# Optimization experiments

Hardware: AMD Instinct MI355X
Metric: run time of the kernel (lower is better)

The kernel has to match this reference:

```python
import jax, jax.numpy as jnp
import numpy as np

D_MODEL = 1024
N_HEADS = 16
HEAD_DIM = D_MODEL // N_HEADS


def setup_inputs() -> dict:
    key = jax.random.key(0)
    k1, k2, k3 = jax.random.split(key, 3)
    x = jax.random.normal(k1, (2, 2048, D_MODEL), dtype=jnp.float32)
    w_qkv = jax.random.normal(k2, (3 * D_MODEL, D_MODEL), dtype=jnp.float32) * 0.02
    w_out = jax.random.normal(k3, (D_MODEL, D_MODEL), dtype=jnp.float32) * 0.02
    return {"x": x, "w_qkv": w_qkv, "w_out": w_out}


def reference(x, w_qkv, w_out):
    B, T, D = x.shape
    H, Hd = N_HEADS, HEAD_DIM
    # QKV projection: Linear stores weight as [out, in] -> '...i,oi->...o'
    qkv = jnp.einsum('bti,oi->bto', x, w_qkv)              # [B, T, 3D]
    # split (3*H, Hs) group-major, chunk into q/k/v of H heads each
    qkv = qkv.reshape(B, T, 3, H, Hd)
    q = jnp.transpose(qkv[:, :, 0], (0, 2, 1, 3))          # [B, H, T, Hd]
    k = jnp.transpose(qkv[:, :, 1], (0, 2, 1, 3))
    v = jnp.transpose(qkv[:, :, 2], (0, 2, 1, 3))
    scale = 1.0 / jnp.sqrt(jnp.asarray(Hd, dtype=x.dtype))
    scores = jnp.einsum('bhqd,bhkd->bhqk', q, k) * scale   # [B, H, T, T]
    causal = jnp.tril(jnp.ones((T, T), dtype=bool))        # [T, T]
    scores = jnp.where(causal[None, None], scores, jnp.asarray(-jnp.inf, dtype=scores.dtype))
    attn = jax.nn.softmax(scores, axis=-1)
    ctx = jnp.einsum('bhqk,bhkd->bhqd', attn, v)           # [B, H, T, Hd]
    ctx = jnp.transpose(ctx, (0, 2, 1, 3)).reshape(B, T, D)
    return jnp.einsum('bti,oi->bto', ctx, w_out)
```

## Files before the change

kernel.cpp:

```cpp
#include <hip/hip_runtime.h>


typedef short short8 __attribute__((ext_vector_type(8)));
typedef float f32x4 __attribute__((ext_vector_type(4)));
typedef unsigned short u16;
typedef unsigned int u32;

#define T_SEQ 2048
#define N_B 2
#define N_H 16
#define HD 64
#define DM 1024
#define TRIPLE 3072

__device__ __forceinline__ u16 f2bf(float f) {
  union { float f; unsigned u; } v;
  v.f = f;
  unsigned r = v.u + 0x7fffu + ((v.u >> 16) & 1u);
  return (u16)(r >> 16);
}

__device__ __forceinline__ float bf2f(u16 x) {
  return __uint_as_float((u32)x << 16);
}

__device__ __forceinline__ u32 cvtpk(float a, float b) {
  u32 r;
  asm("v_cvt_pk_bf16_f32 %0, %1, %2" : "=v"(r) : "v"(a), "v"(b));
  return r;
}

typedef const __attribute__((address_space(1))) void gvoid;
typedef __attribute__((address_space(3))) void lvoid;

__device__ __forceinline__ void g2l16(const void* g, void* l) {
  __builtin_amdgcn_global_load_lds((gvoid*)g, (lvoid*)l, 16, 0, 0);
}

__device__ __forceinline__ void storeC(float* p, float v) { *p = v; }
__device__ __forceinline__ void storeC(u16* p, float v) { *p = f2bf(v); }

__global__ __launch_bounds__(256) void cast_all(const float4* __restrict__ x,
                                                const float4* __restrict__ wq,
                                                const float4* __restrict__ wo,
                                                ushort4* __restrict__ out) {
  int i = blockIdx.x * 256 + threadIdx.x;
  const float4* src;
  int off;
  if (i < 1048576) { src = x; off = 0; }
  else if (i < 1835008) { src = wq; off = 1048576; }
  else { src = wo; off = 1835008; }
  float4 v = src[i - off];
  ushort4 o;
  o.x = f2bf(v.x); o.y = f2bf(v.y); o.z = f2bf(v.z); o.w = f2bf(v.w);
  out[i] = o;
}

__global__ __launch_bounds__(256) void vtrans(const u16* __restrict__ qkv,
                                              u16* __restrict__ vT) {
  const int tid = threadIdx.x;
  const int w = tid >> 6, lane = tid & 63;
  const int ti = lane >> 3, di = lane & 7;
  const int h = blockIdx.y, b = blockIdx.z;
  const int t0 = blockIdx.x * 256 + w * 64 + ti * 8;

  const u16* src = qkv + (size_t)(b * T_SEQ + t0) * TRIPLE + 2 * DM + h * HD + di * 8;
  u32 x[8][4];
#pragma unroll
  for (int e = 0; e < 8; ++e) {
    union { short8 v; u32 u[4]; } cv;
    cv.v = *(const short8*)(src + (size_t)e * TRIPLE);
#pragma unroll
    for (int j = 0; j < 4; ++j) x[e][j] = cv.u[j];
  }
  u32 y[8][4];
#pragma unroll
  for (int a = 0; a < 4; ++a)
#pragma unroll
    for (int j = 0; j < 4; ++j) {
      u32 lo = x[2 * a][j], hi = x[2 * a + 1][j];
      y[2 * a][j] = (lo & 0x0000FFFFu) | (hi << 16);
      y[2 * a + 1][j] = (lo >> 16) | (hi & 0xFFFF0000u);
    }
  u16* dst = vT + ((size_t)(b * N_H + h) * HD + di * 8) * T_SEQ + t0;
#pragma unroll
  for (int dd = 0; dd < 8; ++dd) {
    union { short8 v; u32 u[4]; } cv;
#pragma unroll
    for (int a = 0; a < 4; ++a) cv.u[a] = y[2 * a + (dd & 1)][dd >> 1];
    *(short8*)(dst + (size_t)dd * T_SEQ) = cv.v;
  }
}

template <typename OutT>
__global__ __launch_bounds__(256) void gemm_bt(const u16* __restrict__ A,
                                               const u16* __restrict__ W,
                                               OutT* __restrict__ C,
                                               int M, int N, int K) {
  __shared__ char As[128 * 64 * 2];
  __shared__ char Bs[128 * 64 * 2];
  const int tid = threadIdx.x;
  const int lane = tid & 63, w = tid >> 6;
  const int l15 = lane & 15, l4 = lane >> 4;
  const int m0 = blockIdx.y * 128, n0 = blockIdx.x * 128;
  const int wr = (w >> 1) * 64, wc = (w & 1) * 64;

  const f32x4 zero = {0.f, 0.f, 0.f, 0.f};
  f32x4 acc[4][4];
#pragma unroll
  for (int m = 0; m < 4; ++m)
#pragma unroll
    for (int n = 0; n < 4; ++n) acc[m][n] = zero;

  for (int k0 = 0; k0 < K; k0 += 64) {
#pragma unroll
    for (int i = 0; i < 4; ++i) {
      const int cb = (i * 4 + w) * 64;
      const int c = cb + lane;
      const int row = c >> 3;
      const int ks = ((c & 7) ^ (row & 7)) * 8;
      g2l16(A + (size_t)(m0 + row) * K + k0 + ks, As + (size_t)cb * 16);
      g2l16(W + (size_t)(n0 + row) * K + k0 + ks, Bs + (size_t)cb * 16);
    }
    __syncthreads();

#pragma unroll
    for (int kk = 0; kk < 2; ++kk) {
      short8 a[4], b[4];
#pragma unroll
      for (int m = 0; m < 4; ++m) {
        int row = wr + m * 16 + l15;
        int slot = (kk * 4 + l4) ^ (row & 7);
        a[m] = *(const short8*)(As + row * 128 + slot * 16);
      }
#pragma unroll
      for (int n = 0; n < 4; ++n) {
        int row = wc + n * 16 + l15;
        int slot = (kk * 4 + l4) ^ (row & 7);
        b[n] = *(const short8*)(Bs + row * 128 + slot * 16);
      }
#pragma unroll
      for (int m = 0; m < 4; ++m)
#pragma unroll
        for (int n = 0; n < 4; ++n)
          acc[m][n] = __builtin_amdgcn_mfma_f32_16x16x32_bf16(a[m], b[n], acc[m][n], 0, 0, 0);
    }
    __syncthreads();
  }

#pragma unroll
  for (int m = 0; m < 4; ++m)
#pragma unroll
    for (int n = 0; n < 4; ++n)
#pragma unroll
      for (int r = 0; r < 4; ++r) {
        int row = m0 + wr + m * 16 + l4 * 4 + r;
        int col = n0 + wc + n * 16 + l15;
        storeC(C + (size_t)row * N + col, acc[m][n][r]);
      }
}

__global__ __launch_bounds__(256) void attn_fwd(const u16* __restrict__ qkv,
                                                const u16* __restrict__ vT,
                                                u16* __restrict__ ctx) {
  __shared__ char Ks[3][8192];
  __shared__ char Vs[3][8192];
  __shared__ char Pl[4][2048];

  const int tid = threadIdx.x;
  const int lane = tid & 63, w = tid >> 6;
  const int l15 = lane & 15, l4 = lane >> 4;
  const int g = blockIdx.x;
  const int p = blockIdx.y;
  const int h = g & 15, b = g >> 4;
  const int q0A = 64 * p, q0B = 64 * (31 - p);

  const float c_log2 = 0.18033688011112042f;
  short8 qa2[2][2];
#pragma unroll
  for (int ps = 0; ps < 2; ++ps) {
    const int qq0 = ps ? q0B : q0A;
    const u16* qp = qkv + (size_t)(b * T_SEQ + qq0 + w * 16 + l15) * TRIPLE + h * HD;
#pragma unroll
    for (int kk = 0; kk < 2; ++kk) {
      short8 raw = *(const short8*)(qp + kk * 32 + l4 * 8);
      union { short8 v; u32 w4[4]; } qq;
#pragma unroll
      for (int j = 0; j < 4; ++j)
        qq.w4[j] = cvtpk(bf2f((u16)raw[2 * j]) * c_log2,
                         bf2f((u16)raw[2 * j + 1]) * c_log2);
      qa2[ps][kk] = qq.v;
    }
  }

  const int r0 = tid >> 3, c0 = tid & 7;
  const int swz = (c0 ^ (r0 & 7)) << 3;
  const u16* kbase = qkv + (size_t)(b * T_SEQ + r0) * TRIPLE + DM + h * HD + swz;
  const u16* vbase = vT + ((size_t)g * HD + r0) * T_SEQ + swz;

#define STAGE(kt_, buf_)                                                        \
  {                                                                             \
    g2l16(kbase + (size_t)((kt_) * 64) * TRIPLE, Ks[buf_] + tid * 16);          \
    g2l16(kbase + (size_t)((kt_) * 64 + 32) * TRIPLE, Ks[buf_] + tid * 16 + 4096); \
    g2l16(vbase + (u32)((kt_) * 64), Vs[buf_] + tid * 16);                      \
    g2l16(vbase + (size_t)32 * T_SEQ + (u32)((kt_) * 64), Vs[buf_] + tid * 16 + 4096); \
  }

  char* Plb = Pl[w];

  const f32x4 zero = {0.f, 0.f, 0.f, 0.f};
  f32x4 o[4];
#pragma unroll
  for (int nt = 0; nt < 4; ++nt) o[nt] = zero;
  float mr = -INFINITY, lr = 0.f;
  short8 qa0 = qa2[0][0], qa1 = qa2[0][1];
  int q0 = q0A;

  STAGE(0, 0);
  {
    const int kt1 = (1 <= p) ? 1 : 31;
    STAGE(kt1, 1);
  }
  asm volatile("s_waitcnt vmcnt(4)\n\ts_barrier" ::: "memory");

  int cur = 0;
  for (int i = 0;; ++i) {
    const int kt = (i <= p) ? i : 32 - i;

    if (i + 2 <= 32) {
      const int kt2 = (i + 2 <= p) ? i + 2 : 30 - i;
      int sb = cur - 1;
      if (sb < 0) sb = 2;
      STAGE(kt2, sb);
    }

    const int k0 = kt * 64;
    if (k0 <= q0 + w * 16) {
      f32x4 s[4];
#pragma unroll
      for (int mt = 0; mt < 4; ++mt) s[mt] = zero;
      __builtin_amdgcn_s_setprio(1);
#pragma unroll
      for (int mt = 0; mt < 4; ++mt) {
        int row = mt * 16 + l15;
        int slot0 = l4 ^ (row & 7);
        short8 kb0 = *(const short8*)(Ks[cur] + row * 128 + slot0 * 16);
        s[mt] = __builtin_amdgcn_mfma_f32_16x16x32_bf16(kb0, qa0, s[mt], 0, 0, 0);
        int slot1 = (4 + l4) ^ (row & 7);
        short8 kb1 = *(const short8*)(Ks[cur] + row * 128 + slot1 * 16);
        s[mt] = __builtin_amdgcn_mfma_f32_16x16x32_bf16(kb1, qa1, s[mt], 0, 0, 0);
      }
      __builtin_amdgcn_s_setprio(0);

      if (i == p || i == p + 1) {
        const int qrow = q0 + w * 16 + l15;
#pragma unroll
        for (int mt = 0; mt < 4; ++mt)
#pragma unroll
          for (int r = 0; r < 4; ++r) {
            int key = k0 + mt * 16 + l4 * 4 + r;
            if (key > qrow) s[mt][r] = -INFINITY;
          }
      }

      float mx = fmaxf(fmaxf(fmaxf(s[0][0], s[0][1]), fmaxf(s[0][2], s[0][3])),
                       fmaxf(fmaxf(s[1][0], s[1][1]), fmaxf(s[1][2], s[1][3])));
      mx = fmaxf(mx, fmaxf(fmaxf(fmaxf(s[2][0], s[2][1]), fmaxf(s[2][2], s[2][3])),
                           fmaxf(fmaxf(s[3][0], s[3][1]), fmaxf(s[3][2], s[3][3]))));
      mx = fmaxf(mx, __shfl_xor(mx, 16));
      mx = fmaxf(mx, __shfl_xor(mx, 32));
      if (!__all(mx - mr <= 8.0f)) {
        float mn = fmaxf(mr, mx);
        float fr = exp2f(mr - mn);
        lr *= fr;
#pragma unroll
        for (int r = 0; r < 4; ++r) {
          float frq = __shfl(fr, l4 * 4 + r);
#pragma unroll
          for (int nt = 0; nt < 4; ++nt) o[nt][r] *= frq;
        }
        mr = mn;
      }
      float ps = 0.f;
#pragma unroll
      for (int mt = 0; mt < 4; ++mt)
#pragma unroll
        for (int r = 0; r < 4; ++r) {
          float pv = exp2f(s[mt][r] - mr);
          s[mt][r] = pv;
          ps += pv;
        }
      lr += ps;

#pragma unroll
      for (int mt = 0; mt < 4; ++mt) {
        uint2 pw;
        pw.x = cvtpk(s[mt][0], s[mt][1]);
        pw.y = cvtpk(s[mt][2], s[mt][3]);
        int slot = ((mt * 2 + (l4 >> 1)) ^ (l15 & 7));
        *(uint2*)(Plb + l15 * 128 + (slot << 4) + ((l4 & 1) << 3)) = pw;
      }

      __builtin_amdgcn_s_setprio(1);
#pragma unroll
      for (int kk = 0; kk < 2; ++kk) {
        short8 pa = *(const short8*)(Plb + l15 * 128 + (((kk * 4 + l4) ^ (l15 & 7)) << 4));
#pragma unroll
        for (int nt = 0; nt < 4; ++nt) {
          int d = nt * 16 + l15;
          int slot = (kk * 4 + l4) ^ (l15 & 7);
          short8 vb = *(const short8*)(Vs[cur] + d * 128 + slot * 16);
          o[nt] = __builtin_amdgcn_mfma_f32_16x16x32_bf16(pa, vb, o[nt], 0, 0, 0);
        }
      }
      __builtin_amdgcn_s_setprio(0);
    }

    if (i == p || i == 32) {
      lr += __shfl_xor(lr, 16);
      lr += __shfl_xor(lr, 32);
#pragma unroll
      for (int r = 0; r < 4; ++r) {
        float lrq = __shfl(lr, l4 * 4 + r);
        float inv = __builtin_amdgcn_rcpf(lrq);
        size_t t = (size_t)(b * T_SEQ + q0 + w * 16 + l4 * 4 + r);
#pragma unroll
        for (int nt = 0; nt < 4; ++nt)
          ctx[t * DM + h * HD + nt * 16 + l15] = f2bf(o[nt][r] * inv);
      }
      if (i == 32) break;
#pragma unroll
      for (int nt = 0; nt < 4; ++nt) o[nt] = zero;
      mr = -INFINITY; lr = 0.f;
      qa0 = qa2[1][0]; qa1 = qa2[1][1];
      q0 = q0B;
    }

    if (i == 31)
      asm volatile("s_waitcnt vmcnt(0)\n\ts_barrier" ::: "memory");
    else
      asm volatile("s_waitcnt vmcnt(4)\n\ts_barrier" ::: "memory");
    cur = (cur == 2) ? 0 : cur + 1;
  }
#undef STAGE
}

extern "C" void kernel_launch(void* const* d_in, const int* in_sizes, int n_in,
                              void* d_out, int out_size, void* d_ws, size_t ws_size,
                              hipStream_t stream) {
  const float* x = (const float*)d_in[0];
  const float* wqkv = (const float*)d_in[1];
  const float* wout = (const float*)d_in[2];
  float* out = (float*)d_out;
  char* ws = (char*)d_ws;

  u16* xb    = (u16*)(ws);
  u16* wqkvb = (u16*)(ws + 8u * 1024 * 1024);
  u16* woutb = (u16*)(ws + 14u * 1024 * 1024);
  u16* qkvb  = (u16*)(ws + 16u * 1024 * 1024);
  u16* ctxb  = (u16*)(ws + 40u * 1024 * 1024);
  u16* vTb   = (u16*)(ws + 48u * 1024 * 1024);

  cast_all<<<8192, 256, 0, stream>>>((const float4*)x, (const float4*)wqkv,
                                     (const float4*)wout, (ushort4*)xb);

  gemm_bt<u16><<<dim3(24, 32), 256, 0, stream>>>(xb, wqkvb, qkvb, 4096, 3072, 1024);

  vtrans<<<dim3(8, N_H, N_B), 256, 0, stream>>>(qkvb, vTb);

  attn_fwd<<<dim3(32, 16), 256, 0, stream>>>(qkvb, vTb, ctxb);

  gemm_bt<float><<<dim3(8, 32), 256, 0, stream>>>(ctxb, woutb, out, 4096, 1024, 1024);
}
```

Baseline: 130.2 us.

## Double attention tile to 128 queries and keys with 512-thread blocks

Enlarges the attention work tile from 64 to 128 query rows per pass and 128 keys per stage, using 8 waves per block and half the grid in the pair dimension. Each staged K/V tile is now reused by twice as many waves and the loop runs half as many iterations with fewer barriers. The cost is roughly double the LDS per block, more score registers per wave, fewer blocks (less occupancy), and more work wasted at the diagonal tile under the causal mask.

```diff
diff --git a/kernel.cpp b/kernel.cpp
--- a/kernel.cpp
+++ b/kernel.cpp
@@ -160,12 +160,12 @@
       }
 }
 
-__global__ __launch_bounds__(256) void attn_fwd(const u16* __restrict__ qkv,
+__global__ __launch_bounds__(512) void attn_fwd(const u16* __restrict__ qkv,
                                                 const u16* __restrict__ vT,
                                                 u16* __restrict__ ctx) {
-  __shared__ char Ks[3][8192];
-  __shared__ char Vs[3][8192];
-  __shared__ char Pl[4][2048];
+  __shared__ char Ks[3][16384];
+  __shared__ char Vs[3][16384];
+  __shared__ char Pl[8][4096];
 
   const int tid = threadIdx.x;
   const int lane = tid & 63, w = tid >> 6;
@@ -173,7 +173,7 @@
   const int g = blockIdx.x;
   const int p = blockIdx.y;
   const int h = g & 15, b = g >> 4;
-  const int q0A = 64 * p, q0B = 64 * (31 - p);
+  const int q0A = 128 * p, q0B = 128 * (15 - p);
 
   const float c_log2 = 0.18033688011112042f;
   short8 qa2[2][2];
@@ -193,17 +193,21 @@
     }
   }
 
-  const int r0 = tid >> 3, c0 = tid & 7;
-  const int swz = (c0 ^ (r0 & 7)) << 3;
-  const u16* kbase = qkv + (size_t)(b * T_SEQ + r0) * TRIPLE + DM + h * HD + swz;
-  const u16* vbase = vT + ((size_t)g * HD + r0) * T_SEQ + swz;
-
-#define STAGE(kt_, buf_)                                                        \
-  {                                                                             \
-    g2l16(kbase + (size_t)((kt_) * 64) * TRIPLE, Ks[buf_] + tid * 16);          \
-    g2l16(kbase + (size_t)((kt_) * 64 + 32) * TRIPLE, Ks[buf_] + tid * 16 + 4096); \
-    g2l16(vbase + (u32)((kt_) * 64), Vs[buf_] + tid * 16);                      \
-    g2l16(vbase + (size_t)32 * T_SEQ + (u32)((kt_) * 64), Vs[buf_] + tid * 16 + 4096); \
+  const int kr = tid >> 3;
+  const int kswz = ((tid & 7) ^ (kr & 7)) << 3;
+  const u16* kbase = qkv + (size_t)(b * T_SEQ + kr) * TRIPLE + DM + h * HD + kswz;
+  const int vd = tid >> 4;
+  const int vswz = ((tid & 15) ^ (vd & 7)) << 3;
+  const u16* vbase = vT + ((size_t)g * HD + vd) * T_SEQ + vswz;
+
+#define STAGE(kt_, buf_)                                                      \
+  {                                                                           \
+    g2l16(kbase + (size_t)((kt_) * 128) * TRIPLE, Ks[buf_] + tid * 16);       \
+    g2l16(kbase + (size_t)((kt_) * 128 + 64) * TRIPLE,                        \
+          Ks[buf_] + (512 + tid) * 16);                                       \
+    g2l16(vbase + (u32)((kt_) * 128), Vs[buf_] + tid * 16);                   \
+    g2l16(vbase + (size_t)32 * T_SEQ + (u32)((kt_) * 128),                    \
+          Vs[buf_] + (512 + tid) * 16);                                       \
   }
 
   char* Plb = Pl[w];
@@ -218,30 +222,30 @@
 
   STAGE(0, 0);
   {
-    const int kt1 = (1 <= p) ? 1 : 31;
+    const int kt1 = (1 <= p) ? 1 : 15;
     STAGE(kt1, 1);
   }
   asm volatile("s_waitcnt vmcnt(4)\n\ts_barrier" ::: "memory");
 
   int cur = 0;
   for (int i = 0;; ++i) {
-    const int kt = (i <= p) ? i : 32 - i;
-
-    if (i + 2 <= 32) {
-      const int kt2 = (i + 2 <= p) ? i + 2 : 30 - i;
+    const int kt = (i <= p) ? i : 16 - i;
+
+    if (i + 2 <= 16) {
+      const int kt2 = (i + 2 <= p) ? (i + 2) : 14 - i;
       int sb = cur - 1;
       if (sb < 0) sb = 2;
       STAGE(kt2, sb);
     }
 
-    const int k0 = kt * 64;
+    const int k0 = kt * 128;
     if (k0 <= q0 + w * 16) {
-      f32x4 s[4];
-#pragma unroll
-      for (int mt = 0; mt < 4; ++mt) s[mt] = zero;
+      f32x4 s[8];
+#pragma unroll
+      for (int mt = 0; mt < 8; ++mt) s[mt] = zero;
       __builtin_amdgcn_s_setprio(1);
 #pragma unroll
-      for (int mt = 0; mt < 4; ++mt) {
+      for (int mt = 0; mt < 8; ++mt) {
         int row = mt * 16 + l15;
         int slot0 = l4 ^ (row & 7);
         short8 kb0 = *(const short8*)(Ks[cur] + row * 128 + slot0 * 16);
@@ -255,7 +259,7 @@
       if (i == p || i == p + 1) {
         const int qrow = q0 + w * 16 + l15;
 #pragma unroll
-        for (int mt = 0; mt < 4; ++mt)
+        for (int mt = 0; mt < 8; ++mt)
 #pragma unroll
           for (int r = 0; r < 4; ++r) {
             int key = k0 + mt * 16 + l4 * 4 + r;
@@ -263,10 +267,16 @@
           }
       }
 
-      float mx = fmaxf(fmaxf(fmaxf(s[0][0], s[0][1]), fmaxf(s[0][2], s[0][3])),
-                       fmaxf(fmaxf(s[1][0], s[1][1]), fmaxf(s[1][2], s[1][3])));
-      mx = fmaxf(mx, fmaxf(fmaxf(fmaxf(s[2][0], s[2][1]), fmaxf(s[2][2], s[2][3])),
-                           fmaxf(fmaxf(s[3][0], s[3][1]), fmaxf(s[3][2], s[3][3]))));
+      float tA = fmaxf(s[0][0], s[1][0]), tB = fmaxf(s[0][1], s[1][1]);
+      float tC = fmaxf(s[0][2], s[1][2]), tD = fmaxf(s[0][3], s[1][3]);
+#pragma unroll
+      for (int mt = 2; mt < 8; ++mt) {
+        tA = fmaxf(tA, s[mt][0]);
+        tB = fmaxf(tB, s[mt][1]);
+        tC = fmaxf(tC, s[mt][2]);
+        tD = fmaxf(tD, s[mt][3]);
+      }
+      float mx = fmaxf(fmaxf(tA, tB), fmaxf(tC, tD));
       mx = fmaxf(mx, __shfl_xor(mx, 16));
       mx = fmaxf(mx, __shfl_xor(mx, 32));
       if (!__all(mx - mr <= 8.0f)) {
@@ -283,7 +293,7 @@
       }
       float ps = 0.f;
 #pragma unroll
-      for (int mt = 0; mt < 4; ++mt)
+      for (int mt = 0; mt < 8; ++mt)
 #pragma unroll
         for (int r = 0; r < 4; ++r) {
           float pv = exp2f(s[mt][r] - mr);
@@ -293,30 +303,31 @@
       lr += ps;
 
 #pragma unroll
-      for (int mt = 0; mt < 4; ++mt) {
+      for (int mt = 0; mt < 8; ++mt) {
         uint2 pw;
         pw.x = cvtpk(s[mt][0], s[mt][1]);
         pw.y = cvtpk(s[mt][2], s[mt][3]);
-        int slot = ((mt * 2 + (l4 >> 1)) ^ (l15 & 7));
-        *(uint2*)(Plb + l15 * 128 + (slot << 4) + ((l4 & 1) << 3)) = pw;
+        int sc = (mt * 2 + (l4 >> 1)) ^ (l15 & 7);
+        *(uint2*)(Plb + l15 * 256 + (sc << 4) + ((l4 & 1) << 3)) = pw;
       }
 
       __builtin_amdgcn_s_setprio(1);
 #pragma unroll
-      for (int kk = 0; kk < 2; ++kk) {
-        short8 pa = *(const short8*)(Plb + l15 * 128 + (((kk * 4 + l4) ^ (l15 & 7)) << 4));
+      for (int kk = 0; kk < 4; ++kk) {
+        int pc = (kk * 4 + l4) ^ (l15 & 7);
+        short8 pa = *(const short8*)(Plb + l15 * 256 + (pc << 4));
 #pragma unroll
         for (int nt = 0; nt < 4; ++nt) {
           int d = nt * 16 + l15;
-          int slot = (kk * 4 + l4) ^ (l15 & 7);
-          short8 vb = *(const short8*)(Vs[cur] + d * 128 + slot * 16);
+          int vc = (kk * 4 + l4) ^ (d & 7);
+          short8 vb = *(const short8*)(Vs[cur] + d * 256 + (vc << 4));
           o[nt] = __builtin_amdgcn_mfma_f32_16x16x32_bf16(pa, vb, o[nt], 0, 0, 0);
         }
       }
       __builtin_amdgcn_s_setprio(0);
     }
 
-    if (i == p || i == 32) {
+    if (i == p || i == 16) {
       lr += __shfl_xor(lr, 16);
       lr += __shfl_xor(lr, 32);
 #pragma unroll
@@ -328,7 +339,7 @@
         for (int nt = 0; nt < 4; ++nt)
           ctx[t * DM + h * HD + nt * 16 + l15] = f2bf(o[nt][r] * inv);
       }
-      if (i == 32) break;
+      if (i == 16) break;
 #pragma unroll
       for (int nt = 0; nt < 4; ++nt) o[nt] = zero;
       mr = -INFINITY; lr = 0.f;
@@ -336,7 +347,7 @@
       q0 = q0B;
     }
 
-    if (i == 31)
+    if (i == 15)
       asm volatile("s_waitcnt vmcnt(0)\n\ts_barrier" ::: "memory");
     else
       asm volatile("s_waitcnt vmcnt(4)\n\ts_barrier" ::: "memory");
@@ -368,7 +379,7 @@
 
   vtrans<<<dim3(8, N_H, N_B), 256, 0, stream>>>(qkvb, vTb);
 
-  attn_fwd<<<dim3(32, 16), 256, 0, stream>>>(qkvb, vTb, ctxb);
+  attn_fwd<<<dim3(32, 8), 512, 0, stream>>>(qkvb, vTb, ctxb);
 
   gemm_bt<float><<<dim3(8, 32), 256, 0, stream>>>(ctxb, woutb, out, 4096, 1024, 1024);
 }
```

After: 121.6 us. -6.6%, faster.
